# Kernel optimization log

Hardware: AMD Instinct MI355X
Metric: run time of the kernel (lower is better)

The kernel has to match this reference:

```python
import jax, jax.numpy as jnp
import numpy as np

N_NODES = 100000
N_EDGES = 1600000
D_IN = 64
D_OUT = 64
NEG_SLOPE = 0.01  # torch F.leaky_relu default


def setup_inputs() -> dict:
    key = jax.random.key(0)
    k1, k2, k3, k4, k5 = jax.random.split(key, 5)
    feat = jax.random.normal(k1, (N_NODES, D_IN), dtype=jnp.float32)
    src = jax.random.randint(k2, (N_EDGES,), 0, N_NODES)
    dst = jax.random.randint(k3, (N_EDGES,), 0, N_NODES)
    # fc_neigh weight (stored [in, out]) and bias, Glorot-ish scale
    W = jax.random.normal(k4, (D_IN, D_OUT), dtype=jnp.float32) / jnp.sqrt(jnp.float32(D_IN))
    b = jax.random.normal(k5, (D_OUT,), dtype=jnp.float32) * 0.01
    return {"feat": feat, "src": src, "dst": dst, "W": W, "b": b}


def reference(feat, src, dst, W, b):
    # DGL SAGEConv 'gcn' aggregator:
    #   h_v = (sum_{u->v} feat_u + feat_v) / (in_deg(v) + 1)
    #   out = h @ W + b ; then module applies leaky_relu
    msg_sum = jax.ops.segment_sum(feat[src], dst, num_segments=N_NODES)   # [N, D_IN]
    deg = jax.ops.segment_sum(jnp.ones((src.shape[0],), feat.dtype), dst,
                              num_segments=N_NODES)                        # [N]
    h = (msg_sum + feat) / (deg[:, None] + 1.0)
    out = h @ W + b
    return jnp.where(out >= 0, out, NEG_SLOPE * out)
```

## Files before the change

kernel.cpp:

```cpp
#include <hip/hip_runtime.h>

#define N_NODES 100000
#define N_EDGES 1600000
#define D 64
#define CAP 64


__global__ __launch_bounds__(256) void binfill(
    const int* __restrict__ src,
    const int* __restrict__ dst,
    int*       __restrict__ cursor,
    int*       __restrict__ slots)
{
    const int e = blockIdx.x * blockDim.x + threadIdx.x;
    if (e >= N_EDGES) return;
    const int d = dst[e];
    const int s = src[e];
    const int pos = atomicAdd(&cursor[d], 1);
    if (pos < CAP) slots[(size_t)d * CAP + pos] = s;
}

__global__ __launch_bounds__(256) void gather_gemm(
    const float* __restrict__ feat,
    const int*   __restrict__ cursor,
    const int*   __restrict__ slots,
    const float* __restrict__ W,
    const float* __restrict__ b,
    float*       __restrict__ out)
{
    __shared__ float Wl[D * D];
    __shared__ float bl[D];
    __shared__ float hl[4][D];
    for (int i = threadIdx.x; i < D * D; i += blockDim.x) Wl[i] = W[i];
    if (threadIdx.x < D) bl[threadIdx.x] = b[threadIdx.x];
    __syncthreads();

    const int lane = threadIdx.x & 63;
    const int w    = threadIdx.x >> 6;
    const int waveId = blockIdx.x * 4 + w;
    const int nWaves = gridDim.x * 4;

    for (int node = waveId; node < N_NODES; node += nWaves) {
        const size_t fbase = (size_t)node * D;
        const int deg = cursor[node];
        const int cnt = deg < CAP ? deg : CAP;
        const int ids = slots[(size_t)node * CAP + lane];

        float a0 = feat[fbase + lane];
        float a1 = 0.f, a2 = 0.f, a3 = 0.f;
        int j = 0;
        for (; j + 4 <= cnt; j += 4) {
            const int s0 = __shfl(ids, j,     64);
            const int s1 = __shfl(ids, j + 1, 64);
            const int s2 = __shfl(ids, j + 2, 64);
            const int s3 = __shfl(ids, j + 3, 64);
            a0 += feat[(size_t)s0 * D + lane];
            a1 += feat[(size_t)s1 * D + lane];
            a2 += feat[(size_t)s2 * D + lane];
            a3 += feat[(size_t)s3 * D + lane];
        }
        for (; j < cnt; ++j) {
            const int s0 = __shfl(ids, j, 64);
            a0 += feat[(size_t)s0 * D + lane];
        }
        const float h = ((a0 + a1) + (a2 + a3)) / (float)(deg + 1);

        hl[w][lane] = h;

        float acc0 = bl[lane];
        float acc1 = 0.f;
        #pragma unroll
        for (int i = 0; i < D; i += 2) {
            acc0 = fmaf(hl[w][i],     Wl[i * D + lane],       acc0);
            acc1 = fmaf(hl[w][i + 1], Wl[(i + 1) * D + lane], acc1);
        }
        const float acc = acc0 + acc1;
        out[fbase + lane] = acc >= 0.f ? acc : 0.01f * acc;
    }
}

extern "C" void kernel_launch(void* const* d_in, const int* in_sizes, int n_in,
                              void* d_out, int out_size, void* d_ws, size_t ws_size,
                              hipStream_t stream) {
    const float* feat = (const float*)d_in[0];
    const int*   src  = (const int*)d_in[1];
    const int*   dst  = (const int*)d_in[2];
    const float* W    = (const float*)d_in[3];
    const float* b    = (const float*)d_in[4];
    float*       out  = (float*)d_out;

    int* cursor = (int*)d_ws;
    int* slots  = cursor + N_NODES;

    hipMemsetAsync(cursor, 0, (size_t)N_NODES * sizeof(int), stream);

    binfill<<<(N_EDGES + 255) / 256, 256, 0, stream>>>(src, dst, cursor, slots);

    gather_gemm<<<2048, 256, 0, stream>>>(feat, cursor, slots, W, b, out);
}
```

Baseline: 287.4 us.

## Gather neighbor features in bf16 and partition bin-fill atomics by XCD

Adds a pass that converts feat to a bf16 copy, so each neighbor gather reads half the bytes. The bin-fill kernel becomes a grid-stride loop where each XCD-mapped block group handles only edges whose destination falls in its node range, keeping atomics local to one die. The gather loop is unrolled to 8 accumulators, and nontemporal loads and stores are used for streaming data. This costs an extra conversion pass, makes every block scan all edges in binfill, and loses precision in the aggregated neighbor features.

Result: no change. 281.8 us (-1.9%).

```diff
diff --git a/kernel.cpp b/kernel.cpp
--- a/kernel.cpp
+++ b/kernel.cpp
@@ -4,29 +4,61 @@
 #define N_EDGES 1600000
 #define D 64
 #define CAP 64
+#define NXCD 8
+#define NODES_PER_XCD (N_NODES / NXCD)
 
 
-__global__ __launch_bounds__(256) void binfill(
+__global__ __launch_bounds__(256) void feat_to_bf16(
+    const float* __restrict__ feat, ushort* __restrict__ featb)
+{
+    const int i = blockIdx.x * blockDim.x + threadIdx.x;
+    const int n4 = N_NODES * D / 4;
+    if (i >= n4) return;
+    const float4 v = ((const float4*)feat)[i];
+    const float vv[4] = {v.x, v.y, v.z, v.w};
+    ushort4 o;
+    ushort oo[4];
+    #pragma unroll
+    for (int k = 0; k < 4; ++k) {
+        const uint u = __float_as_uint(vv[k]);
+        oo[k] = (ushort)((u + 0x7FFFu + ((u >> 16) & 1u)) >> 16);
+    }
+    o.x = oo[0]; o.y = oo[1]; o.z = oo[2]; o.w = oo[3];
+    ((ushort4*)featb)[i] = o;
+}
+
+__global__ __launch_bounds__(256) void binfill_part(
     const int* __restrict__ src,
     const int* __restrict__ dst,
     int*       __restrict__ cursor,
     int*       __restrict__ slots)
 {
-    const int e = blockIdx.x * blockDim.x + threadIdx.x;
-    if (e >= N_EDGES) return;
-    const int d = dst[e];
-    const int s = src[e];
-    const int pos = atomicAdd(&cursor[d], 1);
-    if (pos < CAP) slots[(size_t)d * CAP + pos] = s;
+    const int xcd  = blockIdx.x & (NXCD - 1);
+    const int blk  = blockIdx.x >> 3;
+    const int nblk = gridDim.x >> 3;
+    const int lo   = xcd * NODES_PER_XCD;
+    const int hi   = lo + NODES_PER_XCD;
+
+    const int tid    = blk * blockDim.x + threadIdx.x;
+    const int stride = nblk * blockDim.x;
+    for (int e = tid; e < N_EDGES; e += stride) {
+        const int d = __builtin_nontemporal_load(&dst[e]);
+        const int s = __builtin_nontemporal_load(&src[e]);
+        if (d >= lo && d < hi) {
+            const int pos = atomicAdd(&cursor[d], 1);
+            if (pos < CAP) slots[(size_t)d * CAP + pos] = s;
+        }
+    }
 }
 
 __global__ __launch_bounds__(256) void gather_gemm(
-    const float* __restrict__ feat,
-    const int*   __restrict__ cursor,
-    const int*   __restrict__ slots,
-    const float* __restrict__ W,
-    const float* __restrict__ b,
-    float*       __restrict__ out)
+    const float*  __restrict__ feat,
+    const ushort* __restrict__ featb,
+    const int*    __restrict__ cursor,
+    const int*    __restrict__ slots,
+    const float*  __restrict__ W,
+    const float*  __restrict__ b,
+    float*        __restrict__ out)
 {
     __shared__ float Wl[D * D];
     __shared__ float bl[D];
@@ -44,26 +76,43 @@
         const size_t fbase = (size_t)node * D;
         const int deg = cursor[node];
         const int cnt = deg < CAP ? deg : CAP;
-        const int ids = slots[(size_t)node * CAP + lane];
+        const int ids = __builtin_nontemporal_load(&slots[(size_t)node * CAP + lane]);
 
-        float a0 = feat[fbase + lane];
-        float a1 = 0.f, a2 = 0.f, a3 = 0.f;
+        float a0 = __builtin_nontemporal_load(&feat[fbase + lane]);
+        float a1 = 0.f, a2 = 0.f, a3 = 0.f, a4 = 0.f, a5 = 0.f, a6 = 0.f, a7 = 0.f;
         int j = 0;
-        for (; j + 4 <= cnt; j += 4) {
+        for (; j + 8 <= cnt; j += 8) {
             const int s0 = __shfl(ids, j,     64);
             const int s1 = __shfl(ids, j + 1, 64);
             const int s2 = __shfl(ids, j + 2, 64);
             const int s3 = __shfl(ids, j + 3, 64);
-            a0 += feat[(size_t)s0 * D + lane];
-            a1 += feat[(size_t)s1 * D + lane];
-            a2 += feat[(size_t)s2 * D + lane];
-            a3 += feat[(size_t)s3 * D + lane];
+            const int s4 = __shfl(ids, j + 4, 64);
+            const int s5 = __shfl(ids, j + 5, 64);
+            const int s6 = __shfl(ids, j + 6, 64);
+            const int s7 = __shfl(ids, j + 7, 64);
+            const ushort u0 = featb[(size_t)s0 * D + lane];
+            const ushort u1 = featb[(size_t)s1 * D + lane];
+            const ushort u2 = featb[(size_t)s2 * D + lane];
+            const ushort u3 = featb[(size_t)s3 * D + lane];
+            const ushort u4 = featb[(size_t)s4 * D + lane];
+            const ushort u5 = featb[(size_t)s5 * D + lane];
+            const ushort u6 = featb[(size_t)s6 * D + lane];
+            const ushort u7 = featb[(size_t)s7 * D + lane];
+            a0 += __uint_as_float((uint)u0 << 16);
+            a1 += __uint_as_float((uint)u1 << 16);
+            a2 += __uint_as_float((uint)u2 << 16);
+            a3 += __uint_as_float((uint)u3 << 16);
+            a4 += __uint_as_float((uint)u4 << 16);
+            a5 += __uint_as_float((uint)u5 << 16);
+            a6 += __uint_as_float((uint)u6 << 16);
+            a7 += __uint_as_float((uint)u7 << 16);
         }
         for (; j < cnt; ++j) {
             const int s0 = __shfl(ids, j, 64);
-            a0 += feat[(size_t)s0 * D + lane];
+            a0 += __uint_as_float((uint)featb[(size_t)s0 * D + lane] << 16);
         }
-        const float h = ((a0 + a1) + (a2 + a3)) / (float)(deg + 1);
+        const float h = (((a0 + a1) + (a2 + a3)) + ((a4 + a5) + (a6 + a7)))
+                        / (float)(deg + 1);
 
         hl[w][lane] = h;
 
@@ -75,7 +124,7 @@
             acc1 = fmaf(hl[w][i + 1], Wl[(i + 1) * D + lane], acc1);
         }
         const float acc = acc0 + acc1;
-        out[fbase + lane] = acc >= 0.f ? acc : 0.01f * acc;
+        __builtin_nontemporal_store(acc >= 0.f ? acc : 0.01f * acc, &out[fbase + lane]);
     }
 }
 
@@ -89,12 +138,17 @@
     const float* b    = (const float*)d_in[4];
     float*       out  = (float*)d_out;
 
-    int* cursor = (int*)d_ws;
-    int* slots  = cursor + N_NODES;
+    char* ws = (char*)d_ws;
+    int*    slots  = (int*)ws;
+    int*    cursor = (int*)(ws + (size_t)N_NODES * CAP * 4);
+    ushort* featb  = (ushort*)(ws + (size_t)N_NODES * CAP * 4
+                                  + (size_t)N_NODES * 4);
 
     hipMemsetAsync(cursor, 0, (size_t)N_NODES * sizeof(int), stream);
 
-    binfill<<<(N_EDGES + 255) / 256, 256, 0, stream>>>(src, dst, cursor, slots);
+    feat_to_bf16<<<(N_NODES * D / 4 + 255) / 256, 256, 0, stream>>>(feat, featb);
 
-    gather_gemm<<<2048, 256, 0, stream>>>(feat, cursor, slots, W, b, out);
+    binfill_part<<<1024, 256, 0, stream>>>(src, dst, cursor, slots);
+
+    gather_gemm<<<2048, 256, 0, stream>>>(feat, featb, cursor, slots, W, b, out);
 }
```
